# Optimization experiments

Measured on AMD Instinct MI355X. Metric: run time of the kernel, lower is better.

## Reference

```python
import jax, jax.numpy as jnp
import numpy as np

EMB_DIM = 512
R_DIM = 64
B, S = 8, 2048


def _lowrank_params(key):
    k1, k2, k3, k4 = jax.random.split(key, 4)
    s1 = 1.0 / np.sqrt(EMB_DIM)
    s2 = 1.0 / np.sqrt(R_DIM)
    w1 = jax.random.uniform(k1, (EMB_DIM, R_DIM), jnp.float32, -s1, s1)
    b1 = jax.random.uniform(k2, (R_DIM,), jnp.float32, -s1, s1)
    w2 = jax.random.uniform(k3, (R_DIM, EMB_DIM), jnp.float32, -s2, s2)
    b2 = jax.random.uniform(k4, (EMB_DIM,), jnp.float32, -s2, s2)
    return w1, b1, w2, b2


def setup_inputs() -> dict:
    key = jax.random.key(0)
    kx, km, kq, kk, kv = jax.random.split(key, 5)
    x = jax.random.normal(kx, (B, S, EMB_DIM), jnp.float32)
    attention_mask = jax.random.randint(km, (B, S), 0, 2, jnp.int32)
    q_w1, q_b1, q_w2, q_b2 = _lowrank_params(kq)
    k_w1, k_b1, k_w2, k_b2 = _lowrank_params(kk)
    v_w1, v_b1, v_w2, v_b2 = _lowrank_params(kv)
    return dict(x=x, attention_mask=attention_mask,
                q_w1=q_w1, q_b1=q_b1, q_w2=q_w2, q_b2=q_b2,
                k_w1=k_w1, k_b1=k_b1, k_w2=k_w2, k_b2=k_b2,
                v_w1=v_w1, v_b1=v_b1, v_w2=v_w2, v_b2=v_b2)


def _proj(x, w1, b1, w2, b2):
    # low-rank projection: emb -> r -> emb (two stacked Linears, no nonlinearity)
    return (x @ w1 + b1) @ w2 + b2


def reference(x, attention_mask,
              q_w1, q_b1, q_w2, q_b2,
              k_w1, k_b1, k_w2, k_b2,
              v_w1, v_b1, v_w2, v_b2):
    q = _proj(x, q_w1, q_b1, q_w2, q_b2)   # [B,S,E]
    k = _proj(x, k_w1, k_b1, k_w2, k_b2)   # [B,S,E]
    v = _proj(x, v_w1, v_b1, v_w2, v_b2)   # [B,S,E]
    scale = EMB_DIM ** (-0.5)
    scores = jnp.einsum('bse,bte->bst', q, k) * scale  # [B,S,S]
    m = attention_mask.astype(jnp.float32)
    scores = scores * m[:, :, None] * m[:, None, :]
    temp = jnp.einsum('bst,bte->bse', scores, v)       # [B,S,E]
    out = jax.nn.softmax(temp, axis=-1)                # softmax AFTER second bmm (non-standard)
    return out, q
```

## Files before the change

kernel.cpp:

```cpp
#include <hip/hip_runtime.h>
#include <hip/hip_bf16.h>

#define SCALE 0.044194173824159216f

typedef float f32x4 __attribute__((ext_vector_type(4)));
typedef __bf16 bf16x8 __attribute__((ext_vector_type(8)));

static __device__ __forceinline__ unsigned short f2bf(float f){
  unsigned u = __builtin_bit_cast(unsigned, f);
  u += 0x7fffu + ((u >> 16) & 1u);
  return (unsigned short)(u >> 16);
}

__global__ __launch_bounds__(256) void kA(const float* __restrict__ w1q, const float* __restrict__ w1k,
    const float* __restrict__ w1v, const float* __restrict__ w2q, const float* __restrict__ b2q,
    const float* __restrict__ w2k, const float* __restrict__ b2k,
    unsigned short* __restrict__ W1T, unsigned short* __restrict__ W2qT, float* __restrict__ Pm){
  const int bid = blockIdx.x, t = threadIdx.x;
  if (bid < 64){
    #pragma unroll
    for (int s = 0; s < 8; s++){
      int id = s*16384 + bid*256 + t;
      if (id < 192*512){
        int n = id >> 9, k = id & 511;
        int p = n >> 6, c = n & 63;
        const float* w1 = (p==0)? w1q : ((p==1)? w1k : w1v);
        W1T[id] = f2bf(w1[k*64 + c]);
      } else {
        int j = id - 192*512;
        int e = j >> 6, r = j & 63;
        W2qT[j] = f2bf(w2q[r*512 + e]);
      }
    }
  } else {
    int id = (bid - 64)*256 + t;
    if (id >= 65*65) return;
    int i = id / 65, j = id - i*65;
    const float* qi = (i < 64)? (w2q + i*512) : b2q;
    const float* kj = (j < 64)? (w2k + j*512) : b2k;
    float s = 0.f;
    for (int e = 0; e < 512; e += 4){
      float4 a = *(const float4*)(qi + e);
      float4 b = *(const float4*)(kj + e);
      s += a.x*b.x; s += a.y*b.y; s += a.z*b.z; s += a.w*b.w;
    }
    Pm[id] = s * SCALE;
  }
}

__global__ __launch_bounds__(256) void kB(const float* __restrict__ x, const unsigned short* __restrict__ W1T,
    const float* __restrict__ b1q, const float* __restrict__ b1k, const float* __restrict__ b1v,
    const int* __restrict__ mask,
    unsigned short* __restrict__ Hq, float* __restrict__ part){
  __shared__ __attribute__((aligned(16))) char smem[33792];
  unsigned short (*Ax)[40] = (unsigned short(*)[40])smem;
  unsigned short (*Bt)[40] = (unsigned short(*)[40])(smem + 5120);
  float (*ak)[66] = (float(*)[66])smem;
  float (*av)[66] = (float(*)[66])(smem + 16896);
  const int t = threadIdx.x;
  const int lane = t & 63, wave = t >> 6;
  const int l15 = lane & 15, lg = lane >> 4, ks = lg * 8;
  const int r0 = blockIdx.x * 64;
  f32x4 acc[12];
  #pragma unroll
  for (int j = 0; j < 12; j++) acc[j] = (f32x4){0.f,0.f,0.f,0.f};
  for (int k0 = 0; k0 < 512; k0 += 32){
    #pragma unroll
    for (int s = 0; s < 2; s++){
      int i = t + 256*s;
      int r = i >> 3, kq = (i & 7) * 4;
      float4 v = *(const float4*)(x + (size_t)(r0 + r)*512 + k0 + kq);
      ushort4 pk; pk.x = f2bf(v.x); pk.y = f2bf(v.y); pk.z = f2bf(v.z); pk.w = f2bf(v.w);
      *(ushort4*)&Ax[r][kq] = pk;
    }
    #pragma unroll
    for (int s = 0; s < 3; s++){
      int i = t + 256*s;
      int n = i >> 2, kq = (i & 3) * 8;
      *(uint4*)&Bt[n][kq] = *(const uint4*)(W1T + n*512 + k0 + kq);
    }
    __syncthreads();
    const int arow = (wave << 4) | l15;
    bf16x8 af = *(const bf16x8*)&Ax[arow][ks];
    #pragma unroll
    for (int j = 0; j < 12; j++){
      bf16x8 bf = *(const bf16x8*)&Bt[j*16 + l15][ks];
      acc[j] = __builtin_amdgcn_mfma_f32_16x16x32_bf16(af, bf, acc[j], 0, 0, 0);
    }
    __syncthreads();
  }
  int rowl[4]; float mrow[4];
  #pragma unroll
  for (int rg = 0; rg < 4; rg++){
    rowl[rg] = (wave << 4) + (lg << 2) + rg;
    mrow[rg] = (float)mask[r0 + rowl[rg]];
  }
  #pragma unroll
  for (int j = 0; j < 4; j++){
    int c = (j << 4) | l15;
    float bias = b1q[c];
    #pragma unroll
    for (int rg = 0; rg < 4; rg++)
      Hq[(size_t)(r0 + rowl[rg])*64 + c] = f2bf(acc[j][rg] + bias);
  }
  #pragma unroll
  for (int j = 0; j < 4; j++){
    int c = (j << 4) | l15;
    float bias = b1k[c];
    #pragma unroll
    for (int rg = 0; rg < 4; rg++)
      ak[rowl[rg]][c] = (acc[4 + j][rg] + bias) * mrow[rg];
  }
  #pragma unroll
  for (int j = 0; j < 4; j++){
    int c = (j << 4) | l15;
    float bias = b1v[c];
    #pragma unroll
    for (int rg = 0; rg < 4; rg++)
      av[rowl[rg]][c] = acc[8 + j][rg] + bias;
  }
  if (t < 64){ ak[t][64] = (float)mask[r0 + t]; av[t][64] = 1.f; }
  __syncthreads();
  if (t < 169){
    int tj = t / 13, ti = t - tj*13;
    int i0 = ti * 5, j0 = tj * 5;
    float pacc[5][5];
    #pragma unroll
    for (int a = 0; a < 5; a++)
      #pragma unroll
      for (int v = 0; v < 5; v++) pacc[a][v] = 0.f;
    for (int r = 0; r < 64; r++){
      float a[5], v[5];
      #pragma unroll
      for (int ii = 0; ii < 5; ii++) a[ii] = ak[r][i0 + ii];
      #pragma unroll
      for (int jj = 0; jj < 5; jj++) v[jj] = av[r][j0 + jj];
      #pragma unroll
      for (int ii = 0; ii < 5; ii++)
        #pragma unroll
        for (int jj = 0; jj < 5; jj++) pacc[ii][jj] += a[ii] * v[jj];
    }
    float* pout = part + (size_t)blockIdx.x * 4228;
    #pragma unroll
    for (int ii = 0; ii < 5; ii++)
      #pragma unroll
      for (int jj = 0; jj < 5; jj++)
        pout[(i0 + ii)*65 + (j0 + jj)] = pacc[ii][jj];
  }
}

__global__ __launch_bounds__(256) void kCX(const float* __restrict__ part, const float* __restrict__ Pm,
    const float* __restrict__ w2v, const float* __restrict__ b2v,
    unsigned short* __restrict__ GtA, float* __restrict__ Gbias){
  __shared__ float Pl[65*66];
  __shared__ float Atl[4228];
  __shared__ float T1l[65*66];
  const int t = threadIdx.x;
  const int b = blockIdx.x >> 3, ec = (blockIdx.x & 7) << 6;
  for (int id = t; id < 4225; id += 256){
    int i = id / 65, j = id - i*65;
    Pl[i*66 + j] = Pm[id];
  }
  const float* pb = part + (size_t)b*32*4228;
  for (int q = t; q < 1056; q += 256){
    f32x4 s0 = (f32x4){0.f,0.f,0.f,0.f}, s1 = s0, s2 = s0, s3 = s0;
    #pragma unroll
    for (int ch = 0; ch < 32; ch += 4){
      s0 += *(const f32x4*)(pb + (size_t)ch*4228     + q*4);
      s1 += *(const f32x4*)(pb + (size_t)(ch+1)*4228 + q*4);
      s2 += *(const f32x4*)(pb + (size_t)(ch+2)*4228 + q*4);
      s3 += *(const f32x4*)(pb + (size_t)(ch+3)*4228 + q*4);
    }
    *(f32x4*)&Atl[q*4] = (s0 + s1) + (s2 + s3);
  }
  if (t == 0){
    float s = 0.f;
    #pragma unroll
    for (int ch = 0; ch < 32; ch++) s += pb[(size_t)ch*4228 + 4224];
    Atl[4224] = s;
  }
  __syncthreads();
  if (t < 169){
    int tj = t / 13, ti = t - tj*13;
    int i0 = ti * 5, j0 = tj * 5;
    float acc[5][5];
    #pragma unroll
    for (int a = 0; a < 5; a++)
      #pragma unroll
      for (int v = 0; v < 5; v++) acc[a][v] = 0.f;
    for (int k = 0; k < 65; k++){
      float a[5], vv[5];
      #pragma unroll
      for (int ii = 0; ii < 5; ii++) a[ii] = Pl[(i0 + ii)*66 + k];
      #pragma unroll
      for (int jj = 0; jj < 5; jj++) vv[jj] = Atl[k*65 + j0 + jj];
      #pragma unroll
      for (int ii = 0; ii < 5; ii++)
        #pragma unroll
        for (int jj = 0; jj < 5; jj++) acc[ii][jj] += a[ii] * vv[jj];
    }
    #pragma unroll
    for (int ii = 0; ii < 5; ii++)
      #pragma unroll
      for (int jj = 0; jj < 5; jj++) T1l[(i0 + ii)*66 + (j0 + jj)] = acc[ii][jj];
  }
  __syncthreads();
  for (int id = t; id < 4096; id += 256){
    int j = id >> 6, c = id & 63;
    Pl[j*66 + c] = w2v[j*512 + ec + c];
  }
  __syncthreads();
  if (t < 169){
    int tj = t / 13, ti = t - tj*13;
    int i0 = ti * 5, j0 = tj * 5;
    float acc[5][5];
    #pragma unroll
    for (int a = 0; a < 5; a++)
      #pragma unroll
      for (int v = 0; v < 5; v++) acc[a][v] = 0.f;
    for (int k = 0; k < 64; k++){
      float a[5], vv[5];
      #pragma unroll
      for (int ii = 0; ii < 5; ii++) a[ii] = T1l[(i0 + ii)*66 + k];
      #pragma unroll
      for (int jj = 0; jj < 5; jj++) vv[jj] = Pl[k*66 + j0 + jj];
      #pragma unroll
      for (int ii = 0; ii < 5; ii++)
        #pragma unroll
        for (int jj = 0; jj < 5; jj++) acc[ii][jj] += a[ii] * vv[jj];
    }
    #pragma unroll
    for (int ii = 0; ii < 5; ii++){
      int r = i0 + ii;
      float t64 = T1l[r*66 + 64];
      #pragma unroll
      for (int jj = 0; jj < 5; jj++){
        int ej = j0 + jj;
        if (ej < 64){
          int e = ec + ej;
          float s = acc[ii][jj] + t64 * b2v[e];
          if (r < 64) GtA[((size_t)b*512 + e)*64 + r] = f2bf(s);
          else        Gbias[b*512 + e] = s;
        }
      }
    }
  }
}

__global__ __launch_bounds__(256) void kD(const unsigned short* __restrict__ Hq, const unsigned short* __restrict__ W2qT,
    const unsigned short* __restrict__ GtA, const float* __restrict__ Gbias, const float* __restrict__ b2q,
    const int* __restrict__ mask, float* __restrict__ out, float* __restrict__ qout){
  const int t = threadIdx.x, lane = t & 63, wave = t >> 6;
  const int b = blockIdx.x >> 5, rc = (blockIdx.x & 31) << 6;
  const int l15 = lane & 15, lg = lane >> 4, ks = lg * 8;
  const size_t gr0 = (size_t)b*2048 + rc;
  const int arow = (wave << 4) | l15;
  const unsigned short* arp = Hq + (gr0 + arow)*64 + ks;
  bf16x8 a0 = *(const bf16x8*)arp;
  bf16x8 a1 = *(const bf16x8*)(arp + 32);
  const unsigned short* Bsrc = GtA + (size_t)b*512*64;
  f32x4 acc[32];
  #pragma unroll
  for (int f = 0; f < 32; f++) acc[f] = (f32x4){0.f,0.f,0.f,0.f};
  #pragma unroll
  for (int f = 0; f < 32; f++){
    int col = (f << 4) | l15;
    bf16x8 b0 = *(const bf16x8*)(Bsrc + col*64 + ks);
    bf16x8 b1 = *(const bf16x8*)(Bsrc + col*64 + 32 + ks);
    acc[f] = __builtin_amdgcn_mfma_f32_16x16x32_bf16(a0, b0, acc[f], 0, 0, 0);
    acc[f] = __builtin_amdgcn_mfma_f32_16x16x32_bf16(a1, b1, acc[f], 0, 0, 0);
  }
  #pragma unroll
  for (int f = 0; f < 32; f++){
    float gbv = Gbias[(b << 9) | (f << 4) | l15];
    #pragma unroll
    for (int rg = 0; rg < 4; rg++) acc[f][rg] += gbv;
  }
  #pragma unroll
  for (int rg = 0; rg < 4; rg++){
    int row = rc + (wave << 4) + (lg << 2) + rg;
    float m = (float)mask[b*2048 + row];
    float mx = -3.4e38f;
    #pragma unroll
    for (int f = 0; f < 32; f++){
      float v = acc[f][rg] * m;
      acc[f][rg] = v;
      mx = fmaxf(mx, v);
    }
    #pragma unroll
    for (int d = 1; d < 16; d <<= 1) mx = fmaxf(mx, __shfl_xor(mx, d, 64));
    float sum = 0.f;
    #pragma unroll
    for (int f = 0; f < 32; f++){
      float ev = __expf(acc[f][rg] - mx);
      acc[f][rg] = ev;
      sum += ev;
    }
    #pragma unroll
    for (int d = 1; d < 16; d <<= 1) sum += __shfl_xor(sum, d, 64);
    float inv = 1.f / sum;
    float* orow = out + ((size_t)b*2048 + row) * 512;
    #pragma unroll
    for (int f = 0; f < 32; f++) orow[(f << 4) | l15] = acc[f][rg] * inv;
  }
  #pragma unroll
  for (int f = 0; f < 32; f++) acc[f] = (f32x4){0.f,0.f,0.f,0.f};
  #pragma unroll
  for (int f = 0; f < 32; f++){
    int col = (f << 4) | l15;
    bf16x8 b0 = *(const bf16x8*)(W2qT + col*64 + ks);
    bf16x8 b1 = *(const bf16x8*)(W2qT + col*64 + 32 + ks);
    acc[f] = __builtin_amdgcn_mfma_f32_16x16x32_bf16(a0, b0, acc[f], 0, 0, 0);
    acc[f] = __builtin_amdgcn_mfma_f32_16x16x32_bf16(a1, b1, acc[f], 0, 0, 0);
  }
  #pragma unroll
  for (int f = 0; f < 32; f++){
    int col = (f << 4) | l15;
    float bias = b2q[col];
    #pragma unroll
    for (int rg = 0; rg < 4; rg++){
      int row = rc + (wave << 4) + (lg << 2) + rg;
      qout[((size_t)b*2048 + row) * 512 + col] = acc[f][rg] + bias;
    }
  }
}

extern "C" void kernel_launch(void* const* d_in, const int* in_sizes, int n_in,
                              void* d_out, int out_size, void* d_ws, size_t ws_size,
                              hipStream_t stream){
  const float* x    = (const float*)d_in[0];
  const int*   mask = (const int*)d_in[1];
  const float* q_w1 = (const float*)d_in[2];
  const float* q_b1 = (const float*)d_in[3];
  const float* q_w2 = (const float*)d_in[4];
  const float* q_b2 = (const float*)d_in[5];
  const float* k_w1 = (const float*)d_in[6];
  const float* k_b1 = (const float*)d_in[7];
  const float* k_w2 = (const float*)d_in[8];
  const float* k_b2 = (const float*)d_in[9];
  const float* v_w1 = (const float*)d_in[10];
  const float* v_b1 = (const float*)d_in[11];
  const float* v_w2 = (const float*)d_in[12];
  const float* v_b2 = (const float*)d_in[13];

  char* ws = (char*)d_ws;
  unsigned short* W1T  = (unsigned short*)(ws + 0);
  unsigned short* W2qT = (unsigned short*)(ws + 196608);
  float*          Pm   = (float*)(ws + 262144);
  unsigned short* Hq   = (unsigned short*)(ws + 279296);
  float*          part = (float*)(ws + 2376448);
  unsigned short* GtA  = (unsigned short*)(ws + 6705920);
  float*          Gbias= (float*)(ws + 7230208);

  float* out  = (float*)d_out;
  float* qout = out + (size_t)8*2048*512;

  kA <<<81,  256, 0, stream>>>(q_w1, k_w1, v_w1, q_w2, q_b2, k_w2, k_b2, W1T, W2qT, Pm);
  kB <<<256, 256, 0, stream>>>(x, W1T, q_b1, k_b1, v_b1, mask, Hq, part);
  kCX<<<64,  256, 0, stream>>>(part, Pm, v_w2, v_b2, GtA, Gbias);
  kD <<<256, 256, 0, stream>>>(Hq, W2qT, GtA, Gbias, q_b2, mask, out, qout);
}
```

Measured before the change: 95.30 us.

## Move W2v multiplication from per-batch reduction kernel into final MFMA kernel

The per-batch combined matrix G = T1·[W2v;b2v] is no longer built in a 64-block reduction kernel. An 8-block kernel now emits only T1 (as bf16, transposed and padded to 80 columns), and the final kernel computes Hq·T1 with MFMA into shared memory and then multiplies by a pre-packed bf16 W2v/b2v matrix padded to K=96. This removes the middle kernel's second GEMM and the GtA/Gbias traffic. In exchange the final kernel does an extra small MFMA stage, a block barrier and a third K-chunk, and T1 gets an additional bf16 rounding step.

```diff
diff --git a/kernel.cpp b/kernel.cpp
--- a/kernel.cpp
+++ b/kernel.cpp
@@ -15,7 +15,9 @@
 __global__ __launch_bounds__(256) void kA(const float* __restrict__ w1q, const float* __restrict__ w1k,
     const float* __restrict__ w1v, const float* __restrict__ w2q, const float* __restrict__ b2q,
     const float* __restrict__ w2k, const float* __restrict__ b2k,
-    unsigned short* __restrict__ W1T, unsigned short* __restrict__ W2qT, float* __restrict__ Pm){
+    const float* __restrict__ w2v, const float* __restrict__ b2v,
+    unsigned short* __restrict__ W1T, unsigned short* __restrict__ W2qT, float* __restrict__ Pm,
+    unsigned short* __restrict__ Wvb){
   const int bid = blockIdx.x, t = threadIdx.x;
   if (bid < 64){
     #pragma unroll
@@ -32,19 +34,27 @@
         W2qT[j] = f2bf(w2q[r*512 + e]);
       }
     }
+  } else if (bid < 81){
+    int id = (bid - 64)*256 + t;
+    if (id < 65*65){
+      int i = id / 65, j = id - i*65;
+      const float* qi = (i < 64)? (w2q + i*512) : b2q;
+      const float* kj = (j < 64)? (w2k + j*512) : b2k;
+      float s = 0.f;
+      for (int e = 0; e < 512; e += 4){
+        float4 a = *(const float4*)(qi + e);
+        float4 b = *(const float4*)(kj + e);
+        s += a.x*b.x + a.y*b.y + a.z*b.z + a.w*b.w;
+      }
+      Pm[id] = s * SCALE;
+    }
   } else {
-    int id = (bid - 64)*256 + t;
-    if (id >= 65*65) return;
-    int i = id / 65, j = id - i*65;
-    const float* qi = (i < 64)? (w2q + i*512) : b2q;
-    const float* kj = (j < 64)? (w2k + j*512) : b2k;
-    float s = 0.f;
-    for (int e = 0; e < 512; e += 4){
-      float4 a = *(const float4*)(qi + e);
-      float4 b = *(const float4*)(kj + e);
-      s += a.x*b.x; s += a.y*b.y; s += a.z*b.z; s += a.w*b.w;
-    }
-    Pm[id] = s * SCALE;
+    int e = (bid - 81)*256 + t;
+    unsigned short* wp = Wvb + e*96;
+    for (int k = 0; k < 64; k++) wp[k] = f2bf(w2v[k*512 + e]);
+    wp[64] = f2bf(b2v[e]);
+    #pragma unroll
+    for (int k = 65; k < 96; k++) wp[k] = 0;
   }
 }
 
@@ -149,14 +159,11 @@
   }
 }
 
-__global__ __launch_bounds__(256) void kCX(const float* __restrict__ part, const float* __restrict__ Pm,
-    const float* __restrict__ w2v, const float* __restrict__ b2v,
-    unsigned short* __restrict__ GtA, float* __restrict__ Gbias){
+__global__ __launch_bounds__(256) void kR2(const float* __restrict__ part, const float* __restrict__ Pm,
+    unsigned short* __restrict__ T1bt, float* __restrict__ T1r64){
   __shared__ float Pl[65*66];
   __shared__ float Atl[4228];
-  __shared__ float T1l[65*66];
-  const int t = threadIdx.x;
-  const int b = blockIdx.x >> 3, ec = (blockIdx.x & 7) << 6;
+  const int t = threadIdx.x, b = blockIdx.x;
   for (int id = t; id < 4225; id += 256){
     int i = id / 65, j = id - i*65;
     Pl[i*66 + j] = Pm[id];
@@ -180,6 +187,8 @@
     Atl[4224] = s;
   }
   __syncthreads();
+  unsigned short* Tb = T1bt + b*5120;
+  float* Tr = T1r64 + b*80;
   if (t < 169){
     int tj = t / 13, ti = t - tj*13;
     int i0 = ti * 5, j0 = tj * 5;
@@ -200,56 +209,30 @@
         for (int jj = 0; jj < 5; jj++) acc[ii][jj] += a[ii] * vv[jj];
     }
     #pragma unroll
-    for (int ii = 0; ii < 5; ii++)
-      #pragma unroll
-      for (int jj = 0; jj < 5; jj++) T1l[(i0 + ii)*66 + (j0 + jj)] = acc[ii][jj];
-  }
-  __syncthreads();
-  for (int id = t; id < 4096; id += 256){
-    int j = id >> 6, c = id & 63;
-    Pl[j*66 + c] = w2v[j*512 + ec + c];
-  }
-  __syncthreads();
-  if (t < 169){
-    int tj = t / 13, ti = t - tj*13;
-    int i0 = ti * 5, j0 = tj * 5;
-    float acc[5][5];
-    #pragma unroll
-    for (int a = 0; a < 5; a++)
-      #pragma unroll
-      for (int v = 0; v < 5; v++) acc[a][v] = 0.f;
-    for (int k = 0; k < 64; k++){
-      float a[5], vv[5];
-      #pragma unroll
-      for (int ii = 0; ii < 5; ii++) a[ii] = T1l[(i0 + ii)*66 + k];
-      #pragma unroll
-      for (int jj = 0; jj < 5; jj++) vv[jj] = Pl[k*66 + j0 + jj];
-      #pragma unroll
-      for (int ii = 0; ii < 5; ii++)
-        #pragma unroll
-        for (int jj = 0; jj < 5; jj++) acc[ii][jj] += a[ii] * vv[jj];
-    }
-    #pragma unroll
     for (int ii = 0; ii < 5; ii++){
-      int r = i0 + ii;
-      float t64 = T1l[r*66 + 64];
+      int i = i0 + ii;
       #pragma unroll
       for (int jj = 0; jj < 5; jj++){
-        int ej = j0 + jj;
-        if (ej < 64){
-          int e = ec + ej;
-          float s = acc[ii][jj] + t64 * b2v[e];
-          if (r < 64) GtA[((size_t)b*512 + e)*64 + r] = f2bf(s);
-          else        Gbias[b*512 + e] = s;
-        }
+        int j = j0 + jj;
+        if (i < 64) Tb[j*64 + i] = f2bf(acc[ii][jj]);
+        else        Tr[j] = acc[ii][jj];
       }
     }
   }
-}
-
-__global__ __launch_bounds__(256) void kD(const unsigned short* __restrict__ Hq, const unsigned short* __restrict__ W2qT,
-    const unsigned short* __restrict__ GtA, const float* __restrict__ Gbias, const float* __restrict__ b2q,
-    const int* __restrict__ mask, float* __restrict__ out, float* __restrict__ qout){
+  if (t < 240){
+    int j = 65 + t/16, i4 = (t & 15) << 2;
+    *(ushort4*)&Tb[j*64 + i4] = (ushort4){0,0,0,0};
+  } else if (t < 255){
+    Tr[65 + (t - 240)] = 0.f;
+  }
+}
+
+__global__ __launch_bounds__(256) void kD2(const unsigned short* __restrict__ Hq,
+    const unsigned short* __restrict__ W2qT, const unsigned short* __restrict__ T1bt,
+    const float* __restrict__ T1r64, const unsigned short* __restrict__ Wvb,
+    const float* __restrict__ b2q, const int* __restrict__ mask,
+    float* __restrict__ out, float* __restrict__ qout){
+  __shared__ __attribute__((aligned(16))) unsigned short t1l[64][104];
   const int t = threadIdx.x, lane = t & 63, wave = t >> 6;
   const int b = blockIdx.x >> 5, rc = (blockIdx.x & 31) << 6;
   const int l15 = lane & 15, lg = lane >> 4, ks = lg * 8;
@@ -258,23 +241,45 @@
   const unsigned short* arp = Hq + (gr0 + arow)*64 + ks;
   bf16x8 a0 = *(const bf16x8*)arp;
   bf16x8 a1 = *(const bf16x8*)(arp + 32);
-  const unsigned short* Bsrc = GtA + (size_t)b*512*64;
+  const unsigned short* Tb = T1bt + b*5120;
+  const float* Tr = T1r64 + b*80;
+  f32x4 acc1[5];
+  #pragma unroll
+  for (int jf = 0; jf < 5; jf++) acc1[jf] = (f32x4){0.f,0.f,0.f,0.f};
+  #pragma unroll
+  for (int jf = 0; jf < 5; jf++){
+    int col = (jf << 4) | l15;
+    bf16x8 b0 = *(const bf16x8*)(Tb + col*64 + ks);
+    bf16x8 b1 = *(const bf16x8*)(Tb + col*64 + 32 + ks);
+    acc1[jf] = __builtin_amdgcn_mfma_f32_16x16x32_bf16(a0, b0, acc1[jf], 0, 0, 0);
+    acc1[jf] = __builtin_amdgcn_mfma_f32_16x16x32_bf16(a1, b1, acc1[jf], 0, 0, 0);
+  }
+  *(ushort4*)&t1l[t >> 2][80 + ((t & 3) << 2)] = (ushort4){0,0,0,0};
+  #pragma unroll
+  for (int jf = 0; jf < 5; jf++){
+    int col = (jf << 4) | l15;
+    float tr = Tr[col];
+    #pragma unroll
+    for (int rg = 0; rg < 4; rg++)
+      t1l[(wave << 4) + (lg << 2) + rg][col] = f2bf(acc1[jf][rg] + tr);
+  }
+  __syncthreads();
+  bf16x8 c0 = *(const bf16x8*)&t1l[arow][ks];
+  bf16x8 c1 = *(const bf16x8*)&t1l[arow][32 + ks];
+  bf16x8 c2 = *(const bf16x8*)&t1l[arow][64 + ks];
   f32x4 acc[32];
   #pragma unroll
   for (int f = 0; f < 32; f++) acc[f] = (f32x4){0.f,0.f,0.f,0.f};
   #pragma unroll
   for (int f = 0; f < 32; f++){
     int col = (f << 4) | l15;
-    bf16x8 b0 = *(const bf16x8*)(Bsrc + col*64 + ks);
-    bf16x8 b1 = *(const bf16x8*)(Bsrc + col*64 + 32 + ks);
-    acc[f] = __builtin_amdgcn_mfma_f32_16x16x32_bf16(a0, b0, acc[f], 0, 0, 0);
-    acc[f] = __builtin_amdgcn_mfma_f32_16x16x32_bf16(a1, b1, acc[f], 0, 0, 0);
-  }
-  #pragma unroll
-  for (int f = 0; f < 32; f++){
-    float gbv = Gbias[(b << 9) | (f << 4) | l15];
-    #pragma unroll
-    for (int rg = 0; rg < 4; rg++) acc[f][rg] += gbv;
+    const unsigned short* wp = Wvb + col*96;
+    bf16x8 b0 = *(const bf16x8*)(wp + ks);
+    bf16x8 b1 = *(const bf16x8*)(wp + 32 + ks);
+    bf16x8 b2 = *(const bf16x8*)(wp + 64 + ks);
+    acc[f] = __builtin_amdgcn_mfma_f32_16x16x32_bf16(c0, b0, acc[f], 0, 0, 0);
+    acc[f] = __builtin_amdgcn_mfma_f32_16x16x32_bf16(c1, b1, acc[f], 0, 0, 0);
+    acc[f] = __builtin_amdgcn_mfma_f32_16x16x32_bf16(c2, b2, acc[f], 0, 0, 0);
   }
   #pragma unroll
   for (int rg = 0; rg < 4; rg++){
@@ -349,14 +354,16 @@
   float*          Pm   = (float*)(ws + 262144);
   unsigned short* Hq   = (unsigned short*)(ws + 279296);
   float*          part = (float*)(ws + 2376448);
-  unsigned short* GtA  = (unsigned short*)(ws + 6705920);
-  float*          Gbias= (float*)(ws + 7230208);
+  unsigned short* Wvb  = (unsigned short*)(ws + 6705920);
+  unsigned short* T1bt = (unsigned short*)(ws + 6804224);
+  float*          T1r64= (float*)(ws + 6886144);
 
   float* out  = (float*)d_out;
   float* qout = out + (size_t)8*2048*512;
 
-  kA <<<81,  256, 0, stream>>>(q_w1, k_w1, v_w1, q_w2, q_b2, k_w2, k_b2, W1T, W2qT, Pm);
+  kA <<<83,  256, 0, stream>>>(q_w1, k_w1, v_w1, q_w2, q_b2, k_w2, k_b2, v_w2, v_b2,
+                               W1T, W2qT, Pm, Wvb);
   kB <<<256, 256, 0, stream>>>(x, W1T, q_b1, k_b1, v_b1, mask, Hq, part);
-  kCX<<<64,  256, 0, stream>>>(part, Pm, v_w2, v_b2, GtA, Gbias);
-  kD <<<256, 256, 0, stream>>>(Hq, W2qT, GtA, Gbias, q_b2, mask, out, qout);
-}
+  kR2<<<8,   256, 0, stream>>>(part, Pm, T1bt, T1r64);
+  kD2<<<256, 256, 0, stream>>>(Hq, W2qT, T1bt, T1r64, Wvb, q_b2, mask, out, qout);
+}
```

Result: no change. 93.65 us (-1.7%).
